# Performance work log

Hardware: AMD Instinct MI355X
Metric: run time of the kernel (lower is better)

Reference implementation:

```python
import jax, jax.numpy as jnp
import numpy as np

B, S, D, H = 4, 2048, 1024, 16  # batch, seq, d_hidden, n_heads


def setup_inputs() -> dict:
    key = jax.random.key(0)
    ks = jax.random.split(key, 7)
    scale = 1.0 / np.sqrt(D)
    return {
        "x": jax.random.normal(ks[0], (B, S, D), dtype=jnp.float32),
        "Wq": jax.random.normal(ks[1], (D, D), dtype=jnp.float32) * scale,
        "bq": jax.random.normal(ks[2], (D,), dtype=jnp.float32) * 0.02,
        "Wk": jax.random.normal(ks[3], (D, D), dtype=jnp.float32) * scale,
        "bk": jax.random.normal(ks[4], (D,), dtype=jnp.float32) * 0.02,
        "Wv": jax.random.normal(ks[5], (D, D), dtype=jnp.float32) * scale,
        "bv": jax.random.normal(ks[6], (D,), dtype=jnp.float32) * 0.02,
    }


def reference(x, Wq, bq, Wk, bk, Wv, bv):
    n_heads = H
    head_dim = D // n_heads

    def proj(inp, W, b):
        # torch nn.Linear: y = x @ W^T + b
        y = jnp.einsum("bsd,ed->bse", inp, W) + b
        # split last dim into (H, Wd) then transpose to (B, H, S, Wd)
        return y.reshape(inp.shape[0], inp.shape[1], n_heads, head_dim).transpose(0, 2, 1, 3)

    q = proj(x, Wq, bq)
    k = proj(x, Wk, bk)
    v = proj(x, Wv, bv)

    # scores: (B, H, S, S)
    scores = jnp.einsum("bhqd,bhkd->bhqk", q, k) / jnp.sqrt(jnp.asarray(head_dim, q.dtype))
    attn = jax.nn.softmax(scores, axis=-1)
    h = jnp.einsum("bhqk,bhkd->bhqd", attn, v)  # (B, H, S, Wd)
    h = h.transpose(0, 2, 1, 3).reshape(x.shape[0], x.shape[1], D)  # merge heads
    return h
```

## Files before the change

### kernel.cpp

```cpp
#include <hip/hip_runtime.h>
#include <hip/hip_bf16.h>

#define B_ 4
#define S_ 2048
#define D_ 1024
#define H_ 16
#define HD 64

typedef __bf16 bf16;
typedef __bf16 bf16x4 __attribute__((ext_vector_type(4)));
typedef __bf16 bf16x8 __attribute__((ext_vector_type(8)));
typedef float f32x4 __attribute__((ext_vector_type(4)));
typedef float f32x16 __attribute__((ext_vector_type(16)));

#define LOG2E 1.4426950408889634f

__device__ inline void gload_lds16(const bf16* g, bf16* l) {
    __builtin_amdgcn_global_load_lds(
        (const __attribute__((address_space(1))) void*)g,
        (__attribute__((address_space(3))) void*)l, 16, 0, 0);
}

__device__ inline int swz(int row, int colb) {
    return row * 64 + ((colb ^ ((row & 7) << 4)) >> 1);
}

__device__ inline unsigned cvt_pk_bf16(float lo, float hi) {
    unsigned r;
    asm("v_cvt_pk_bf16_f32 %0, %1, %2" : "=v"(r) : "v"(lo), "v"(hi));
    return r;
}

__global__ void cast_pack_kernel(const float* __restrict__ x,
                                 const float* __restrict__ Wq,
                                 const float* __restrict__ Wk,
                                 const float* __restrict__ Wv,
                                 bf16* __restrict__ Xb, bf16* __restrict__ Wb) {
    const long XN = (long)B_ * S_ * D_;
    const long WN = (long)D_ * D_;
    long i4 = ((long)blockIdx.x * blockDim.x + threadIdx.x) * 4;
    if (i4 < XN) {
        float4 v = *(const float4*)(x + i4);
        bf16* o = Xb + i4;
        o[0] = (bf16)v.x; o[1] = (bf16)v.y; o[2] = (bf16)v.z; o[3] = (bf16)v.w;
    } else {
        long j = i4 - XN;
        if (j < 3 * WN) {
            int which = (int)(j / WN);
            long jj = j - (long)which * WN;
            const float* src = which == 0 ? Wq : which == 1 ? Wk : Wv;
            float4 v = *(const float4*)(src + jj);
            bf16* o = Wb + j;
            o[0] = (bf16)v.x; o[1] = (bf16)v.y; o[2] = (bf16)v.z; o[3] = (bf16)v.w;
        }
    }
}

#define TM 128
#define TN 256
#define TK 64

__global__ __launch_bounds__(512, 2) void gemm_qkv_kernel(
    const bf16* __restrict__ Xb, const bf16* __restrict__ Wb,
    const float* __restrict__ bq, const float* __restrict__ bk,
    const float* __restrict__ bv,
    bf16* __restrict__ Qg, bf16* __restrict__ Kg, bf16* __restrict__ Vt) {
    __shared__ bf16 SMEM[49152];
    bf16* As = SMEM;
    bf16* Bs = SMEM + 16384;
    const int tid = threadIdx.x;
    const int lane = tid & 63;
    const int wid = tid >> 6;
    const int col = lane & 15, grp = lane >> 4;
    const int wr = wid >> 2, wc = wid & 3;

    const int id = blockIdx.x;
    const int id2 = (id & 7) * 96 + (id >> 3);
    const int m0 = (id2 / 12) * TM;
    const int n0 = (id2 % 12) * TN;

    const int r8 = tid >> 3;
    const int cbs = ((tid & 7) * 16) ^ ((r8 & 7) << 4);
    const bf16* asrc = Xb + (size_t)(m0 + r8) * D_ + (cbs >> 1);
    const bf16* bsrc = Wb + (size_t)(n0 + r8) * D_ + (cbs >> 1);

#define STAGE_A(c, kt, j) \
    gload_lds16(asrc + (size_t)(j) * 64 * D_ + (kt) * TK, As + (c) * 8192 + (j) * 4096 + wid * 512)
#define STAGE_B(c, kt, j) \
    gload_lds16(bsrc + (size_t)(j) * 64 * D_ + (kt) * TK, Bs + (c) * 16384 + (j) * 4096 + wid * 512)

    const f32x4 zf = {0.f, 0.f, 0.f, 0.f};
    f32x4 acc[4][4];
#pragma unroll
    for (int m = 0; m < 4; m++)
#pragma unroll
        for (int n = 0; n < 4; n++) acc[m][n] = zf;

    STAGE_A(0, 0, 0); STAGE_A(0, 0, 1);
    STAGE_B(0, 0, 0); STAGE_B(0, 0, 1); STAGE_B(0, 0, 2); STAGE_B(0, 0, 3);
    asm volatile("s_waitcnt vmcnt(0)");
    __builtin_amdgcn_s_barrier();

    int c = 0;
#pragma unroll 1
    for (int kt = 0; kt < D_ / TK; ++kt) {
        const bf16* Ac = As + c * 8192;
        const bf16* Bc = Bs + c * 16384;
        {
            bf16x8 a[4], b[4];
#pragma unroll
            for (int m = 0; m < 4; m++)
                a[m] = *(const bf16x8*)(Ac + swz(wr * 64 + m * 16 + col, grp * 16));
#pragma unroll
            for (int n = 0; n < 4; n++)
                b[n] = *(const bf16x8*)(Bc + swz(wc * 64 + n * 16 + col, grp * 16));
            if (kt < D_ / TK - 1) {
                STAGE_A(c ^ 1, kt + 1, 0); STAGE_A(c ^ 1, kt + 1, 1);
                STAGE_B(c ^ 1, kt + 1, 0);
            }
            __builtin_amdgcn_s_barrier();
            asm volatile("s_waitcnt lgkmcnt(0)");
            __builtin_amdgcn_sched_barrier(0);
            __builtin_amdgcn_s_setprio(1);
#pragma unroll
            for (int m = 0; m < 4; m++)
#pragma unroll
                for (int n = 0; n < 4; n++)
                    acc[m][n] = __builtin_amdgcn_mfma_f32_16x16x32_bf16(a[m], b[n], acc[m][n], 0, 0, 0);
            __builtin_amdgcn_s_setprio(0);
            __builtin_amdgcn_s_barrier();
        }
        {
            bf16x8 a[4], b[4];
#pragma unroll
            for (int m = 0; m < 4; m++)
                a[m] = *(const bf16x8*)(Ac + swz(wr * 64 + m * 16 + col, 64 + grp * 16));
#pragma unroll
            for (int n = 0; n < 4; n++)
                b[n] = *(const bf16x8*)(Bc + swz(wc * 64 + n * 16 + col, 64 + grp * 16));
            if (kt < D_ / TK - 1) {
                STAGE_B(c ^ 1, kt + 1, 1); STAGE_B(c ^ 1, kt + 1, 2); STAGE_B(c ^ 1, kt + 1, 3);
            }
            __builtin_amdgcn_s_barrier();
            asm volatile("s_waitcnt lgkmcnt(0)");
            __builtin_amdgcn_sched_barrier(0);
            __builtin_amdgcn_s_setprio(1);
#pragma unroll
            for (int m = 0; m < 4; m++)
#pragma unroll
                for (int n = 0; n < 4; n++)
                    acc[m][n] = __builtin_amdgcn_mfma_f32_16x16x32_bf16(a[m], b[n], acc[m][n], 0, 0, 0);
            __builtin_amdgcn_s_setprio(0);
            asm volatile("s_waitcnt vmcnt(0)");
            __builtin_amdgcn_s_barrier();
        }
        c ^= 1;
    }
#undef STAGE_A
#undef STAGE_B

    const int which = n0 >> 10;
    if (which == 2) {
        __syncthreads();
        bf16* Vl = SMEM;
#pragma unroll
        for (int n = 0; n < 4; n++) {
            int dl = wc * 64 + n * 16 + col;
            float bias = bv[(n0 - 2048) + dl];
#pragma unroll
            for (int m = 0; m < 4; m++) {
                bf16x4 pv;
#pragma unroll
                for (int i = 0; i < 4; i++) pv[i] = (bf16)(acc[m][n][i] + bias);
                int sl = wr * 64 + m * 16 + grp * 4;
                *(bf16x4*)(&Vl[dl * 128 + (sl ^ ((dl & 7) << 3))]) = pv;
            }
        }
        __syncthreads();
#pragma unroll
        for (int c0 = 0; c0 < 8; c0++) {
            int cc = c0 * 512 + tid;
            int dl = cc >> 4, s8 = (cc & 15) * 8;
            bf16x8 val = *(const bf16x8*)(&Vl[dl * 128 + (s8 ^ ((dl & 7) << 3))]);
            int s = m0 + s8;
            int b = s >> 11, sl = s & 2047;
            int dglob = (n0 - 2048) + dl;
            int h = dglob >> 6, dd = dglob & 63;
            *(bf16x8*)(&Vt[((size_t)(b * H_ + h) * HD + dd) * S_ + sl]) = val;
        }
    } else {
        const float* bp = which == 0 ? bq : bk;
        bf16* dst = which == 0 ? Qg : Kg;
        const float qsc = which == 0 ? (0.125f * LOG2E) : 1.0f;
#pragma unroll
        for (int n = 0; n < 4; n++) {
            int e = n0 + wc * 64 + n * 16 + col;
            int ee = e & 1023;
            float bias = bp[ee];
            int h = ee >> 6, d = ee & 63;
#pragma unroll
            for (int m = 0; m < 4; m++) {
#pragma unroll
                for (int i = 0; i < 4; i++) {
                    int s = m0 + wr * 64 + m * 16 + grp * 4 + i;
                    int b = s >> 11, sl = s & 2047;
                    dst[((size_t)(b * H_ + h) * S_ + sl) * HD + d] =
                        (bf16)((acc[m][n][i] + bias) * qsc);
                }
            }
        }
    }
}

#define KB 64

__global__ __launch_bounds__(256, 2) void attn_kernel(
    const bf16* __restrict__ Qg, const bf16* __restrict__ Kg,
    const bf16* __restrict__ Vt, float* __restrict__ out) {
    __shared__ bf16 Ks[2][64 * 64];
    __shared__ bf16 Vs[2][64 * 64];
    const int tid = threadIdx.x, lane = tid & 63, wid = tid >> 6;
    const int l31 = lane & 31, hi = lane >> 5;

    const int id = blockIdx.x;
    const int swzid = (id & 7) * 64 + (id >> 3);
    const int bh = swzid >> 3;
    const int q0w = (swzid & 7) * 256 + wid * 64;

    const bf16* Kbase = Kg + (size_t)bh * S_ * HD;
    const bf16* Vbase = Vt + (size_t)bh * HD * S_;

    const int r0 = tid >> 3;
    const int cb = ((tid & 7) * 16) ^ ((r0 & 7) << 4);
    const bf16* ksrc = Kbase + (size_t)r0 * HD + (cb >> 1);
    const bf16* vsrc = Vbase + (size_t)r0 * S_ + (cb >> 1);

#define STAGE(bsel, kv0)                                                       \
    do {                                                                       \
        gload_lds16(ksrc + (size_t)(kv0)*HD,        &Ks[bsel][wid * 512]);     \
        gload_lds16(ksrc + (size_t)((kv0) + 32)*HD, &Ks[bsel][2048 + wid * 512]); \
        gload_lds16(vsrc + (kv0),                   &Vs[bsel][wid * 512]);     \
        gload_lds16(vsrc + 32 * S_ + (kv0),         &Vs[bsel][2048 + wid * 512]); \
    } while (0)

    bf16x8 qa[2][4];
#pragma unroll
    for (int qs = 0; qs < 2; qs++)
#pragma unroll
        for (int ks = 0; ks < 4; ks++)
            qa[qs][ks] = *(const bf16x8*)(Qg + ((size_t)bh * S_ + q0w + qs * 32 + l31) * HD + ks * 16 + hi * 8);

    const f32x16 z16 = {0.f, 0.f, 0.f, 0.f, 0.f, 0.f, 0.f, 0.f,
                        0.f, 0.f, 0.f, 0.f, 0.f, 0.f, 0.f, 0.f};
    f32x16 o[2][2];
    o[0][0] = z16; o[0][1] = z16; o[1][0] = z16; o[1][1] = z16;
    f32x4 ls[2] = {{0.f, 0.f, 0.f, 0.f}, {0.f, 0.f, 0.f, 0.f}};

    int cur = 0;
    STAGE(0, 0);
    __syncthreads();

    for (int t = 0; t < S_ / KB; ++t) {
        if (t < S_ / KB - 1) STAGE(cur ^ 1, (t + 1) * KB);

        f32x16 sc[2][2];
        __builtin_amdgcn_s_setprio(1);
#pragma unroll
        for (int kvt = 0; kvt < 2; kvt++) {
#pragma unroll
            for (int ks = 0; ks < 4; ks++) {
                bf16x8 kb = *(const bf16x8*)(&Ks[cur][swz(kvt * 32 + l31, ks * 32 + hi * 16)]);
                if (ks == 0) {
                    sc[0][kvt] = __builtin_amdgcn_mfma_f32_32x32x16_bf16(kb, qa[0][0], z16, 0, 0, 0);
                    sc[1][kvt] = __builtin_amdgcn_mfma_f32_32x32x16_bf16(kb, qa[1][0], z16, 0, 0, 0);
                } else {
                    sc[0][kvt] = __builtin_amdgcn_mfma_f32_32x32x16_bf16(kb, qa[0][ks], sc[0][kvt], 0, 0, 0);
                    sc[1][kvt] = __builtin_amdgcn_mfma_f32_32x32x16_bf16(kb, qa[1][ks], sc[1][kvt], 0, 0, 0);
                }
            }
        }
        __builtin_amdgcn_s_setprio(0);

        bf16x8 vb[2][4];
#pragma unroll
        for (int kk = 0; kk < 4; kk++)
#pragma unroll
            for (int dt = 0; dt < 2; dt++)
                vb[dt][kk] = *(const bf16x8*)(&Vs[cur][swz(dt * 32 + l31, kk * 32 + hi * 16)]);

#pragma unroll
        for (int qs = 0; qs < 2; qs++) {
            bf16x8 pa[4];
#pragma unroll
            for (int kvt = 0; kvt < 2; kvt++) {
                float p[16];
#pragma unroll
                for (int r = 0; r < 16; r++) p[r] = __builtin_amdgcn_exp2f(sc[qs][kvt][r]);
                f32x4 s0 = {p[0], p[1], p[2], p[3]};
                f32x4 s1 = {p[4], p[5], p[6], p[7]};
                f32x4 s2 = {p[8], p[9], p[10], p[11]};
                f32x4 s3 = {p[12], p[13], p[14], p[15]};
                ls[qs] += (s0 + s1) + (s2 + s3);
#pragma unroll
                for (int b = 0; b < 2; b++) {
                    unsigned A  = cvt_pk_bf16(p[8 * b + 0], p[8 * b + 1]);
                    unsigned Bw = cvt_pk_bf16(p[8 * b + 4], p[8 * b + 5]);
                    unsigned C  = cvt_pk_bf16(p[8 * b + 2], p[8 * b + 3]);
                    unsigned Dw = cvt_pk_bf16(p[8 * b + 6], p[8 * b + 7]);
                    asm("v_permlane32_swap_b32 %0, %1" : "+v"(A), "+v"(Bw));
                    asm("v_permlane32_swap_b32 %0, %1" : "+v"(C), "+v"(Dw));
                    union { unsigned u[4]; bf16x8 v; } pk;
                    pk.u[0] = A; pk.u[1] = C; pk.u[2] = Bw; pk.u[3] = Dw;
                    pa[kvt * 2 + b] = pk.v;
                }
            }

            __builtin_amdgcn_s_setprio(1);
#pragma unroll
            for (int kk = 0; kk < 4; kk++) {
#pragma unroll
                for (int dt = 0; dt < 2; dt++)
                    o[qs][dt] = __builtin_amdgcn_mfma_f32_32x32x16_bf16(vb[dt][kk], pa[kk], o[qs][dt], 0, 0, 0);
            }
            __builtin_amdgcn_s_setprio(0);
        }

        __syncthreads();
        cur ^= 1;
    }

    int b = bh >> 4, h = bh & 15;
#pragma unroll
    for (int qs = 0; qs < 2; qs++) {
        float denom = ls[qs][0] + ls[qs][1] + ls[qs][2] + ls[qs][3];
        denom += __shfl_xor(denom, 32);
        float inv = 1.f / denom;
        int q = q0w + qs * 32 + l31;
        float* obase = out + ((size_t)(b * S_ + q)) * D_ + h * HD;
#pragma unroll
        for (int dt = 0; dt < 2; dt++)
#pragma unroll
            for (int g = 0; g < 4; g++) {
                f32x4 r = {o[qs][dt][4 * g + 0] * inv, o[qs][dt][4 * g + 1] * inv,
                           o[qs][dt][4 * g + 2] * inv, o[qs][dt][4 * g + 3] * inv};
                *(f32x4*)(obase + dt * 32 + 8 * g + 4 * hi) = r;
            }
    }
#undef STAGE
}

extern "C" void kernel_launch(void* const* d_in, const int* in_sizes, int n_in,
                              void* d_out, int out_size, void* d_ws, size_t ws_size,
                              hipStream_t stream) {
    const float* x  = (const float*)d_in[0];
    const float* Wq = (const float*)d_in[1];
    const float* bq = (const float*)d_in[2];
    const float* Wk = (const float*)d_in[3];
    const float* bk = (const float*)d_in[4];
    const float* Wv = (const float*)d_in[5];
    const float* bv = (const float*)d_in[6];
    float* out = (float*)d_out;

    bf16* ws = (bf16*)d_ws;
    bf16* Xb = ws;
    bf16* Wb = Xb + (size_t)B_ * S_ * D_;
    bf16* Qg = Wb + (size_t)3 * D_ * D_;
    bf16* Kg = Qg + (size_t)B_ * S_ * D_;
    bf16* Vt = Kg + (size_t)B_ * S_ * D_;

    hipLaunchKernelGGL(cast_pack_kernel,
                       dim3((B_ * S_ * D_ + 3 * D_ * D_) / (4 * 256)), dim3(256), 0, stream,
                       x, Wq, Wk, Wv, Xb, Wb);
    hipLaunchKernelGGL(gemm_qkv_kernel, dim3(64 * 12), dim3(512), 0, stream,
                       Xb, Wb, bq, bk, bv, Qg, Kg, Vt);
    hipLaunchKernelGGL(attn_kernel, dim3(512), dim3(256), 0, stream,
                       Qg, Kg, Vt, out);
}
```

Baseline: 158.7 us.

## Software-pipeline attention loop: overlap next tile QK^T with current softmax and PV

Restructures the attention main loop so the softmax of tile t runs before the QK^T of tile t+1 is issued, and that QK^T is interleaved with the PV MFMAs of tile t. Two K/V tiles are prefetched up front, and raw s_barrier plus explicit vmcnt waits replace __syncthreads. The aim is to hide exp/convert VALU work behind matrix-core work and to cut barrier stalls. In exchange it adds register pressure from keeping scores and P live across stages, and relies on hand-managed wait counts being correct.

```diff
diff --git a/kernel.cpp b/kernel.cpp
--- a/kernel.cpp
+++ b/kernel.cpp
@@ -213,6 +213,7 @@
 }
 
 #define KB 64
+#define NT (S_ / KB)
 
 __global__ __launch_bounds__(256, 2) void attn_kernel(
     const bf16* __restrict__ Qg, const bf16* __restrict__ Kg,
@@ -250,83 +251,103 @@
         for (int ks = 0; ks < 4; ks++)
             qa[qs][ks] = *(const bf16x8*)(Qg + ((size_t)bh * S_ + q0w + qs * 32 + l31) * HD + ks * 16 + hi * 8);
 
+    STAGE(0, 0);
+    STAGE(1, KB);
+    asm volatile("s_waitcnt vmcnt(4)" ::: "memory");
+    __builtin_amdgcn_s_barrier();
+
     const f32x16 z16 = {0.f, 0.f, 0.f, 0.f, 0.f, 0.f, 0.f, 0.f,
                         0.f, 0.f, 0.f, 0.f, 0.f, 0.f, 0.f, 0.f};
+    f32x16 sc[2][2];
+
+#define QKT(nb)                                                                   \
+    do {                                                                          \
+        __builtin_amdgcn_s_setprio(1);                                            \
+        _Pragma("unroll")                                                         \
+        for (int kvt = 0; kvt < 2; kvt++) {                                       \
+            _Pragma("unroll")                                                     \
+            for (int ks = 0; ks < 4; ks++) {                                      \
+                bf16x8 kb = *(const bf16x8*)(&Ks[nb][swz(kvt * 32 + l31, ks * 32 + hi * 16)]); \
+                if (ks == 0) {                                                    \
+                    sc[0][kvt] = __builtin_amdgcn_mfma_f32_32x32x16_bf16(kb, qa[0][0], z16, 0, 0, 0); \
+                    sc[1][kvt] = __builtin_amdgcn_mfma_f32_32x32x16_bf16(kb, qa[1][0], z16, 0, 0, 0); \
+                } else {                                                          \
+                    sc[0][kvt] = __builtin_amdgcn_mfma_f32_32x32x16_bf16(kb, qa[0][ks], sc[0][kvt], 0, 0, 0); \
+                    sc[1][kvt] = __builtin_amdgcn_mfma_f32_32x32x16_bf16(kb, qa[1][ks], sc[1][kvt], 0, 0, 0); \
+                }                                                                 \
+            }                                                                     \
+        }                                                                         \
+        __builtin_amdgcn_s_setprio(0);                                            \
+    } while (0)
+
+#define SMAX(pa_)                                                                 \
+    do {                                                                          \
+        _Pragma("unroll")                                                         \
+        for (int qs = 0; qs < 2; qs++) {                                          \
+            _Pragma("unroll")                                                     \
+            for (int kvt = 0; kvt < 2; kvt++) {                                   \
+                float p[16];                                                      \
+                _Pragma("unroll")                                                 \
+                for (int r = 0; r < 16; r++) p[r] = __builtin_amdgcn_exp2f(sc[qs][kvt][r]); \
+                f32x4 s0 = {p[0], p[1], p[2], p[3]};                              \
+                f32x4 s1 = {p[4], p[5], p[6], p[7]};                              \
+                f32x4 s2 = {p[8], p[9], p[10], p[11]};                            \
+                f32x4 s3 = {p[12], p[13], p[14], p[15]};                          \
+                ls[qs] += (s0 + s1) + (s2 + s3);                                  \
+                _Pragma("unroll")                                                 \
+                for (int b = 0; b < 2; b++) {                                     \
+                    unsigned A  = cvt_pk_bf16(p[8 * b + 0], p[8 * b + 1]);        \
+                    unsigned Bw = cvt_pk_bf16(p[8 * b + 4], p[8 * b + 5]);        \
+                    unsigned C  = cvt_pk_bf16(p[8 * b + 2], p[8 * b + 3]);        \
+                    unsigned Dw = cvt_pk_bf16(p[8 * b + 6], p[8 * b + 7]);        \
+                    asm("v_permlane32_swap_b32 %0, %1" : "+v"(A), "+v"(Bw));      \
+                    asm("v_permlane32_swap_b32 %0, %1" : "+v"(C), "+v"(Dw));      \
+                    union { unsigned u[4]; bf16x8 v; } pk;                        \
+                    pk.u[0] = A; pk.u[1] = C; pk.u[2] = Bw; pk.u[3] = Dw;         \
+                    pa_[qs][kvt * 2 + b] = pk.v;                                  \
+                }                                                                 \
+            }                                                                     \
+        }                                                                         \
+    } while (0)
+
+#define PVT(cb_)                                                                  \
+    do {                                                                          \
+        __builtin_amdgcn_s_setprio(1);                                            \
+        _Pragma("unroll")                                                         \
+        for (int kk = 0; kk < 4; kk++) {                                          \
+            bf16x8 vb0 = *(const bf16x8*)(&Vs[cb_][swz(l31,      kk * 32 + hi * 16)]); \
+            bf16x8 vb1 = *(const bf16x8*)(&Vs[cb_][swz(32 + l31, kk * 32 + hi * 16)]); \
+            _Pragma("unroll")                                                     \
+            for (int qs = 0; qs < 2; qs++) {                                      \
+                o[qs][0] = __builtin_amdgcn_mfma_f32_32x32x16_bf16(vb0, pa[qs][kk], o[qs][0], 0, 0, 0); \
+                o[qs][1] = __builtin_amdgcn_mfma_f32_32x32x16_bf16(vb1, pa[qs][kk], o[qs][1], 0, 0, 0); \
+            }                                                                     \
+        }                                                                         \
+        __builtin_amdgcn_s_setprio(0);                                            \
+    } while (0)
+
+    QKT(0);
+
     f32x16 o[2][2];
     o[0][0] = z16; o[0][1] = z16; o[1][0] = z16; o[1][1] = z16;
     f32x4 ls[2] = {{0.f, 0.f, 0.f, 0.f}, {0.f, 0.f, 0.f, 0.f}};
 
-    int cur = 0;
-    STAGE(0, 0);
-    __syncthreads();
-
-    for (int t = 0; t < S_ / KB; ++t) {
-        if (t < S_ / KB - 1) STAGE(cur ^ 1, (t + 1) * KB);
-
-        f32x16 sc[2][2];
-        __builtin_amdgcn_s_setprio(1);
-#pragma unroll
-        for (int kvt = 0; kvt < 2; kvt++) {
-#pragma unroll
-            for (int ks = 0; ks < 4; ks++) {
-                bf16x8 kb = *(const bf16x8*)(&Ks[cur][swz(kvt * 32 + l31, ks * 32 + hi * 16)]);
-                if (ks == 0) {
-                    sc[0][kvt] = __builtin_amdgcn_mfma_f32_32x32x16_bf16(kb, qa[0][0], z16, 0, 0, 0);
-                    sc[1][kvt] = __builtin_amdgcn_mfma_f32_32x32x16_bf16(kb, qa[1][0], z16, 0, 0, 0);
-                } else {
-                    sc[0][kvt] = __builtin_amdgcn_mfma_f32_32x32x16_bf16(kb, qa[0][ks], sc[0][kvt], 0, 0, 0);
-                    sc[1][kvt] = __builtin_amdgcn_mfma_f32_32x32x16_bf16(kb, qa[1][ks], sc[1][kvt], 0, 0, 0);
-                }
-            }
-        }
-        __builtin_amdgcn_s_setprio(0);
-
-        bf16x8 vb[2][4];
-#pragma unroll
-        for (int kk = 0; kk < 4; kk++)
-#pragma unroll
-            for (int dt = 0; dt < 2; dt++)
-                vb[dt][kk] = *(const bf16x8*)(&Vs[cur][swz(dt * 32 + l31, kk * 32 + hi * 16)]);
-
-#pragma unroll
-        for (int qs = 0; qs < 2; qs++) {
-            bf16x8 pa[4];
-#pragma unroll
-            for (int kvt = 0; kvt < 2; kvt++) {
-                float p[16];
-#pragma unroll
-                for (int r = 0; r < 16; r++) p[r] = __builtin_amdgcn_exp2f(sc[qs][kvt][r]);
-                f32x4 s0 = {p[0], p[1], p[2], p[3]};
-                f32x4 s1 = {p[4], p[5], p[6], p[7]};
-                f32x4 s2 = {p[8], p[9], p[10], p[11]};
-                f32x4 s3 = {p[12], p[13], p[14], p[15]};
-                ls[qs] += (s0 + s1) + (s2 + s3);
-#pragma unroll
-                for (int b = 0; b < 2; b++) {
-                    unsigned A  = cvt_pk_bf16(p[8 * b + 0], p[8 * b + 1]);
-                    unsigned Bw = cvt_pk_bf16(p[8 * b + 4], p[8 * b + 5]);
-                    unsigned C  = cvt_pk_bf16(p[8 * b + 2], p[8 * b + 3]);
-                    unsigned Dw = cvt_pk_bf16(p[8 * b + 6], p[8 * b + 7]);
-                    asm("v_permlane32_swap_b32 %0, %1" : "+v"(A), "+v"(Bw));
-                    asm("v_permlane32_swap_b32 %0, %1" : "+v"(C), "+v"(Dw));
-                    union { unsigned u[4]; bf16x8 v; } pk;
-                    pk.u[0] = A; pk.u[1] = C; pk.u[2] = Bw; pk.u[3] = Dw;
-                    pa[kvt * 2 + b] = pk.v;
-                }
-            }
-
-            __builtin_amdgcn_s_setprio(1);
-#pragma unroll
-            for (int kk = 0; kk < 4; kk++) {
-#pragma unroll
-                for (int dt = 0; dt < 2; dt++)
-                    o[qs][dt] = __builtin_amdgcn_mfma_f32_32x32x16_bf16(vb[dt][kk], pa[kk], o[qs][dt], 0, 0, 0);
-            }
-            __builtin_amdgcn_s_setprio(0);
-        }
-
-        __syncthreads();
-        cur ^= 1;
+#pragma unroll 1
+    for (int t = 0; t < NT - 1; ++t) {
+        const int cur = t & 1;
+        bf16x8 pa[2][4];
+        SMAX(pa);
+        asm volatile("s_waitcnt vmcnt(0)" ::: "memory");
+        __builtin_amdgcn_s_barrier();
+        QKT(cur ^ 1);
+        PVT(cur);
+        __builtin_amdgcn_s_barrier();
+        if (t < NT - 2) STAGE(cur, (t + 2) * KB);
+    }
+    {
+        bf16x8 pa[2][4];
+        SMAX(pa);
+        PVT(1);
     }
 
     int b = bh >> 4, h = bh & 15;
@@ -347,6 +368,9 @@
             }
     }
 #undef STAGE
+#undef QKT
+#undef SMAX
+#undef PVT
 }
 
 extern "C" void kernel_launch(void* const* d_in, const int* in_sizes, int n_in,
```

Measured after the change: 274.6 us. 1.73x slower.

## Fuse fp32-to-bf16 cast into QKV GEMM via register-staged loads

Applied to the files above, without the earlier changes.

Removes the separate cast/pack kernel and has the QKV GEMM read fp32 x and weights directly from global memory. The fp32 values are held in registers, converted with v_cvt_pk_bf16 and written into the swizzled LDS buffers after the second MFMA phase. This drops one launch and the round trip of writing and re-reading the bf16 copies. In exchange the GEMM now reads twice the bytes per tile (fp32 instead of bf16), re-reads and re-converts the fp32 weights in every block, and replaces async global_load_lds with register staging, which raises register pressure.

```diff
diff --git a/kernel.cpp b/kernel.cpp
--- a/kernel.cpp
+++ b/kernel.cpp
@@ -31,37 +31,31 @@
     return r;
 }
 
-__global__ void cast_pack_kernel(const float* __restrict__ x,
-                                 const float* __restrict__ Wq,
-                                 const float* __restrict__ Wk,
-                                 const float* __restrict__ Wv,
-                                 bf16* __restrict__ Xb, bf16* __restrict__ Wb) {
-    const long XN = (long)B_ * S_ * D_;
-    const long WN = (long)D_ * D_;
-    long i4 = ((long)blockIdx.x * blockDim.x + threadIdx.x) * 4;
-    if (i4 < XN) {
-        float4 v = *(const float4*)(x + i4);
-        bf16* o = Xb + i4;
-        o[0] = (bf16)v.x; o[1] = (bf16)v.y; o[2] = (bf16)v.z; o[3] = (bf16)v.w;
-    } else {
-        long j = i4 - XN;
-        if (j < 3 * WN) {
-            int which = (int)(j / WN);
-            long jj = j - (long)which * WN;
-            const float* src = which == 0 ? Wq : which == 1 ? Wk : Wv;
-            float4 v = *(const float4*)(src + jj);
-            bf16* o = Wb + j;
-            o[0] = (bf16)v.x; o[1] = (bf16)v.y; o[2] = (bf16)v.z; o[3] = (bf16)v.w;
-        }
-    }
+struct f32x8s { float4 lo, hi; };
+__device__ inline f32x8s ld8(const float* p) {
+    f32x8s r;
+    r.lo = *(const float4*)p;
+    r.hi = *(const float4*)(p + 4);
+    return r;
+}
+__device__ inline void wr8(bf16* l, f32x8s v) {
+    union { unsigned u[4]; bf16x8 v8; } pk;
+    pk.u[0] = cvt_pk_bf16(v.lo.x, v.lo.y);
+    pk.u[1] = cvt_pk_bf16(v.lo.z, v.lo.w);
+    pk.u[2] = cvt_pk_bf16(v.hi.x, v.hi.y);
+    pk.u[3] = cvt_pk_bf16(v.hi.z, v.hi.w);
+    *(bf16x8*)l = pk.v8;
 }
 
 #define TM 128
 #define TN 256
 #define TK 64
+#define NKT (D_ / TK)
 
 __global__ __launch_bounds__(512, 2) void gemm_qkv_kernel(
-    const bf16* __restrict__ Xb, const bf16* __restrict__ Wb,
+    const float* __restrict__ x,
+    const float* __restrict__ Wq, const float* __restrict__ Wk,
+    const float* __restrict__ Wv,
     const float* __restrict__ bq, const float* __restrict__ bk,
     const float* __restrict__ bv,
     bf16* __restrict__ Qg, bf16* __restrict__ Kg, bf16* __restrict__ Vt) {
@@ -78,16 +72,13 @@
     const int id2 = (id & 7) * 96 + (id >> 3);
     const int m0 = (id2 / 12) * TM;
     const int n0 = (id2 % 12) * TN;
+    const int which = n0 >> 10;
 
     const int r8 = tid >> 3;
     const int cbs = ((tid & 7) * 16) ^ ((r8 & 7) << 4);
-    const bf16* asrc = Xb + (size_t)(m0 + r8) * D_ + (cbs >> 1);
-    const bf16* bsrc = Wb + (size_t)(n0 + r8) * D_ + (cbs >> 1);
-
-#define STAGE_A(c, kt, j) \
-    gload_lds16(asrc + (size_t)(j) * 64 * D_ + (kt) * TK, As + (c) * 8192 + (j) * 4096 + wid * 512)
-#define STAGE_B(c, kt, j) \
-    gload_lds16(bsrc + (size_t)(j) * 64 * D_ + (kt) * TK, Bs + (c) * 16384 + (j) * 4096 + wid * 512)
+    const float* asrcf = x + (size_t)(m0 + r8) * D_ + (cbs >> 1);
+    const float* wbase = which == 0 ? Wq : which == 1 ? Wk : Wv;
+    const float* bsrcf = wbase + (size_t)((n0 & 1023) + r8) * D_ + (cbs >> 1);
 
     const f32x4 zf = {0.f, 0.f, 0.f, 0.f};
     f32x4 acc[4][4];
@@ -96,16 +87,28 @@
 #pragma unroll
         for (int n = 0; n < 4; n++) acc[m][n] = zf;
 
-    STAGE_A(0, 0, 0); STAGE_A(0, 0, 1);
-    STAGE_B(0, 0, 0); STAGE_B(0, 0, 1); STAGE_B(0, 0, 2); STAGE_B(0, 0, 3);
-    asm volatile("s_waitcnt vmcnt(0)");
-    __builtin_amdgcn_s_barrier();
+    {
+        f32x8s ra0 = ld8(asrcf);
+        f32x8s ra1 = ld8(asrcf + (size_t)64 * D_);
+        f32x8s rb0 = ld8(bsrcf);
+        f32x8s rb1 = ld8(bsrcf + (size_t)64 * D_);
+        f32x8s rb2 = ld8(bsrcf + (size_t)128 * D_);
+        f32x8s rb3 = ld8(bsrcf + (size_t)192 * D_);
+        wr8(As + tid * 8, ra0);
+        wr8(As + 4096 + tid * 8, ra1);
+        wr8(Bs + tid * 8, rb0);
+        wr8(Bs + 4096 + tid * 8, rb1);
+        wr8(Bs + 8192 + tid * 8, rb2);
+        wr8(Bs + 12288 + tid * 8, rb3);
+    }
+    __syncthreads();
 
     int c = 0;
 #pragma unroll 1
-    for (int kt = 0; kt < D_ / TK; ++kt) {
+    for (int kt = 0; kt < NKT; ++kt) {
         const bf16* Ac = As + c * 8192;
         const bf16* Bc = Bs + c * 16384;
+        f32x8s ra0, ra1, rb0, rb1, rb2, rb3;
         {
             bf16x8 a[4], b[4];
 #pragma unroll
@@ -114,9 +117,13 @@
 #pragma unroll
             for (int n = 0; n < 4; n++)
                 b[n] = *(const bf16x8*)(Bc + swz(wc * 64 + n * 16 + col, grp * 16));
-            if (kt < D_ / TK - 1) {
-                STAGE_A(c ^ 1, kt + 1, 0); STAGE_A(c ^ 1, kt + 1, 1);
-                STAGE_B(c ^ 1, kt + 1, 0);
+            if (kt < NKT - 1) {
+                ra0 = ld8(asrcf + (kt + 1) * TK);
+                ra1 = ld8(asrcf + (size_t)64 * D_ + (kt + 1) * TK);
+                rb0 = ld8(bsrcf + (kt + 1) * TK);
+                rb1 = ld8(bsrcf + (size_t)64 * D_ + (kt + 1) * TK);
+                rb2 = ld8(bsrcf + (size_t)128 * D_ + (kt + 1) * TK);
+                rb3 = ld8(bsrcf + (size_t)192 * D_ + (kt + 1) * TK);
             }
             __builtin_amdgcn_s_barrier();
             asm volatile("s_waitcnt lgkmcnt(0)");
@@ -138,9 +145,6 @@
 #pragma unroll
             for (int n = 0; n < 4; n++)
                 b[n] = *(const bf16x8*)(Bc + swz(wc * 64 + n * 16 + col, 64 + grp * 16));
-            if (kt < D_ / TK - 1) {
-                STAGE_B(c ^ 1, kt + 1, 1); STAGE_B(c ^ 1, kt + 1, 2); STAGE_B(c ^ 1, kt + 1, 3);
-            }
             __builtin_amdgcn_s_barrier();
             asm volatile("s_waitcnt lgkmcnt(0)");
             __builtin_amdgcn_sched_barrier(0);
@@ -151,15 +155,22 @@
                 for (int n = 0; n < 4; n++)
                     acc[m][n] = __builtin_amdgcn_mfma_f32_16x16x32_bf16(a[m], b[n], acc[m][n], 0, 0, 0);
             __builtin_amdgcn_s_setprio(0);
-            asm volatile("s_waitcnt vmcnt(0)");
+            if (kt < NKT - 1) {
+                bf16* Ad = As + (c ^ 1) * 8192;
+                bf16* Bd = Bs + (c ^ 1) * 16384;
+                wr8(Ad + tid * 8, ra0);
+                wr8(Ad + 4096 + tid * 8, ra1);
+                wr8(Bd + tid * 8, rb0);
+                wr8(Bd + 4096 + tid * 8, rb1);
+                wr8(Bd + 8192 + tid * 8, rb2);
+                wr8(Bd + 12288 + tid * 8, rb3);
+            }
+            asm volatile("s_waitcnt lgkmcnt(0)");
             __builtin_amdgcn_s_barrier();
         }
         c ^= 1;
     }
-#undef STAGE_A
-#undef STAGE_B
-
-    const int which = n0 >> 10;
+
     if (which == 2) {
         __syncthreads();
         bf16* Vl = SMEM;
@@ -362,17 +373,12 @@
     float* out = (float*)d_out;
 
     bf16* ws = (bf16*)d_ws;
-    bf16* Xb = ws;
-    bf16* Wb = Xb + (size_t)B_ * S_ * D_;
-    bf16* Qg = Wb + (size_t)3 * D_ * D_;
+    bf16* Qg = ws;
     bf16* Kg = Qg + (size_t)B_ * S_ * D_;
     bf16* Vt = Kg + (size_t)B_ * S_ * D_;
 
-    hipLaunchKernelGGL(cast_pack_kernel,
-                       dim3((B_ * S_ * D_ + 3 * D_ * D_) / (4 * 256)), dim3(256), 0, stream,
-                       x, Wq, Wk, Wv, Xb, Wb);
     hipLaunchKernelGGL(gemm_qkv_kernel, dim3(64 * 12), dim3(512), 0, stream,
-                       Xb, Wb, bq, bk, bv, Qg, Kg, Vt);
+                       x, Wq, Wk, Wv, bq, bk, bv, Qg, Kg, Vt);
     hipLaunchKernelGGL(attn_kernel, dim3(512), dim3(256), 0, stream,
                        Qg, Kg, Vt, out);
 }
```

After: 184.5 us. +16.2%, slower.
